# Optimization experiments

Measured on AMD Instinct MI355X. Metric: run time of the kernel, lower is better.

Reference implementation:

```python
import jax, jax.numpy as jnp
import numpy as np

EPS_BN = 1e-5

def _conv1x1(x, w, b):
    # x: [B,C,N], w: [O,C], b: [O] -> [B,O,N]
    return jnp.einsum('oc,bcn->bon', w, x) + b[:, None]

def _bn(x, g, b):
    # BatchNorm1d in training mode: batch stats over (B, N), biased variance
    mu = jnp.mean(x, axis=(0, 2), keepdims=True)
    var = jnp.var(x, axis=(0, 2), keepdims=True)
    return g[:, None] * (x - mu) / jnp.sqrt(var + EPS_BN) + b[:, None]

def _lrelu(x):
    return jnp.where(x >= 0, x, 0.2 * x)

def setup_inputs() -> dict:
    key = jax.random.key(0)
    B, N, S = 4, 16384, 2048
    D1, D2, FINT = 128, 256, 64
    IN, M1, M2 = D1 + D2, 256, 128
    ks = jax.random.split(key, 20)
    def rn(k, shape, scale=1.0):
        return jax.random.normal(k, shape, dtype=jnp.float32) * scale
    return {
        'xyz1': rn(ks[0], (B, 3, N)),
        'xyz2': rn(ks[1], (B, 3, S)),
        'points1': rn(ks[2], (B, D1, N)),
        'points2': rn(ks[3], (B, D2, S)),
        'conv1_w': rn(ks[4], (M1, IN), 0.05), 'conv1_b': rn(ks[5], (M1,), 0.05),
        'bn1_g': jnp.ones((M1,), jnp.float32), 'bn1_b': jnp.zeros((M1,), jnp.float32),
        'conv2_w': rn(ks[6], (M2, M1), 0.05), 'conv2_b': rn(ks[7], (M2,), 0.05),
        'bn2_g': jnp.ones((M2,), jnp.float32), 'bn2_b': jnp.zeros((M2,), jnp.float32),
        'wg_w': rn(ks[8], (FINT, D2), 0.05), 'wg_b': rn(ks[9], (FINT,), 0.05),
        'wg_bn_g': jnp.ones((FINT,), jnp.float32), 'wg_bn_b': jnp.zeros((FINT,), jnp.float32),
        'wx_w': rn(ks[10], (FINT, D1), 0.05), 'wx_b': rn(ks[11], (FINT,), 0.05),
        'wx_bn_g': jnp.ones((FINT,), jnp.float32), 'wx_bn_b': jnp.zeros((FINT,), jnp.float32),
        'psi_w': rn(ks[12], (1, FINT), 0.05), 'psi_b': rn(ks[13], (1,), 0.05),
        'psi_bn_g': jnp.ones((1,), jnp.float32), 'psi_bn_b': jnp.zeros((1,), jnp.float32),
    }

def reference(xyz1, xyz2, points1, points2,
              conv1_w, conv1_b, bn1_g, bn1_b,
              conv2_w, conv2_b, bn2_g, bn2_b,
              wg_w, wg_b, wg_bn_g, wg_bn_b,
              wx_w, wx_b, wx_bn_g, wx_bn_b,
              psi_w, psi_b, psi_bn_g, psi_bn_b):
    x1 = xyz1.transpose(0, 2, 1)        # [B,N,3]
    x2 = xyz2.transpose(0, 2, 1)        # [B,S,3]
    p2 = points2.transpose(0, 2, 1)     # [B,S,D2]
    # squared euclidean distances [B,N,S]
    d = (jnp.sum(x1 * x1, -1)[:, :, None]
         + jnp.sum(x2 * x2, -1)[:, None, :]
         - 2.0 * jnp.einsum('bnc,bsc->bns', x1, x2))
    # 3 smallest distances (torch: full sort + slice [:3])
    neg, idx = jax.lax.top_k(-d, 3)     # idx: [B,N,3]
    d3 = -neg
    recip = 1.0 / (d3 + 1e-8)
    w = recip / jnp.sum(recip, -1, keepdims=True)  # [B,N,3]
    gathered = jax.vmap(lambda p, i: p[i])(p2, idx)  # [B,N,3,D2]
    interp = jnp.einsum('bnkd,bnk->bnd', gathered, w)  # [B,N,D2]
    interp_t = interp.transpose(0, 2, 1)               # [B,D2,N]
    # attention gate: g = interpolated, x = points1
    g1 = _bn(_conv1x1(interp_t, wg_w, wg_b), wg_bn_g, wg_bn_b)
    xx1 = _bn(_conv1x1(points1, wx_w, wx_b), wx_bn_g, wx_bn_b)
    psi = jax.nn.sigmoid(_bn(_conv1x1(_lrelu(g1 + xx1), psi_w, psi_b), psi_bn_g, psi_bn_b))
    p1 = points1 * psi                                  # [B,D1,N]
    new = jnp.concatenate([p1, interp_t], axis=1)       # [B,D1+D2,N]
    new = _lrelu(_bn(_conv1x1(new, conv1_w, conv1_b), bn1_g, bn1_b))
    new = _lrelu(_bn(_conv1x1(new, conv2_w, conv2_b), bn2_g, bn2_b))
    return new
```

## Files before the change

### kernel.cpp

```cpp
#include <hip/hip_runtime.h>
#include <hip/hip_bf16.h>

#define Bq    4
#define NPTS  16384
#define SPTS  2048
#define NCH   8
#define SCH   (SPTS/NCH)
#define CNTF  65536.0f
#define BNEPS 1e-5f

typedef unsigned short u16t;
typedef unsigned int   u32t;
typedef __attribute__((ext_vector_type(8))) short s16x8;
typedef __attribute__((ext_vector_type(4))) float f32x4;

#define AS1(p) ((const __attribute__((address_space(1))) void*)(p))
#define AS3(p) ((__attribute__((address_space(3))) void*)(p))

__device__ __forceinline__ float b2f(u16t u){
  union { u32t i; float f; } v; v.i = ((u32t)u) << 16; return v.f;
}
__device__ __forceinline__ u16t f2b(float f){
  __hip_bfloat16 h = __float2bfloat16(f);
  return *reinterpret_cast<u16t*>(&h);
}
__device__ __forceinline__ float lrelu(float x){ return x >= 0.0f ? x : 0.2f*x; }

#define ST_WG  0
#define ST_WX  128
#define ST_PSI 256
#define ST_BN1 272
#define ST_BN2 784

#define WOFF_C1 0
#define WOFF_C2 98304
#define WOFF_WG 131072
#define WOFF_WX 147456
#define WTOTAL  155648

#define O_STATS  0u
#define O_WB     8192u
#define O_PSIPRE 319488u
#define O_P2T    581632u
#define O_PART   O_P2T
#define O_P1T    4775936u
#define O_INT    21553152u
#define O_H1     55107584u
#define O_PD     O_H1
#define O_PI     (O_H1 + 6291456u)
#define O_IDX3   (O_H1 + 12582912u)
#define O_W3     (O_H1 + 13369344u)
#define O_YG     O_H1
#define O_YX     (O_H1 + 8388608u)
#define O_H2     O_INT

__global__ __launch_bounds__(256) void knn_part_kernel(const float* __restrict__ xyz1, const float* __restrict__ xyz2,
                                                       float* __restrict__ pd, int* __restrict__ pi){
  __shared__ float4 sp[SCH];
  const int b = blockIdx.z;
  const int c = blockIdx.y;
  const int t = threadIdx.x;
  {
    int s = c*SCH + t;
    float x = xyz2[(b*3+0)*SPTS+s];
    float y = xyz2[(b*3+1)*SPTS+s];
    float z = xyz2[(b*3+2)*SPTS+s];
    sp[t] = make_float4(x, y, z, x*x+y*y+z*z);
  }
  __syncthreads();
  const int n = blockIdx.x*256 + t;
  float px = xyz1[(b*3+0)*NPTS+n];
  float py = xyz1[(b*3+1)*NPTS+n];
  float pz = xyz1[(b*3+2)*NPTS+n];
  float s1 = px*px+py*py+pz*pz;
  float d0=3.4e38f, d1=3.4e38f, d2=3.4e38f;
  int   i0=0, i1=0, i2=0;
  for (int s=0; s<SCH; ++s){
    float4 q = sp[s];
    float dot = fmaf(pz, q.z, fmaf(py, q.y, px*q.x));
    float key = (s1 + q.w) - 2.0f*dot;
    if (key < d2){
      int gi = c*SCH + s;
      if (key < d1){
        if (key < d0){ d2=d1; i2=i1; d1=d0; i1=i0; d0=key; i0=gi; }
        else         { d2=d1; i2=i1; d1=key; i1=gi; }
      } else         { d2=key; i2=gi; }
    }
  }
  size_t base = (((size_t)b*NPTS + n)*NCH + c)*3;
  pd[base]=d0; pd[base+1]=d1; pd[base+2]=d2;
  pi[base]=i0; pi[base+1]=i1; pi[base+2]=i2;
}

__global__ __launch_bounds__(256) void knn_merge_kernel(const float* __restrict__ pd, const int* __restrict__ pi,
                                                        int* __restrict__ idx3, float* __restrict__ w3){
  const int p = blockIdx.x*256 + threadIdx.x;
  const float* dp = pd + (size_t)p*NCH*3;
  const int*   ip = pi + (size_t)p*NCH*3;
  float d0=3.4e38f, d1=3.4e38f, d2=3.4e38f;
  int   i0=0, i1=0, i2=0;
  #pragma unroll
  for (int k=0; k<NCH*3; ++k){
    float key = dp[k]; int gi = ip[k];
    if (key < d2){
      if (key < d1){
        if (key < d0){ d2=d1; i2=i1; d1=d0; i1=i0; d0=key; i0=gi; }
        else         { d2=d1; i2=i1; d1=key; i1=gi; }
      } else         { d2=key; i2=gi; }
    }
  }
  float r0=1.0f/(d0+1e-8f), r1=1.0f/(d1+1e-8f), r2=1.0f/(d2+1e-8f);
  float rs = r0+r1+r2;
  size_t base = (size_t)p*3;
  idx3[base]=i0; idx3[base+1]=i1; idx3[base+2]=i2;
  w3[base]=r0/rs; w3[base+1]=r1/rs; w3[base+2]=r2/rs;
}

template<int C, int NN>
__global__ __launch_bounds__(256) void tpose_kernel(const float* __restrict__ src, u16t* __restrict__ dst){
  __shared__ float tile[64][65];
  const int n0 = blockIdx.x * 64;
  const int c0 = blockIdx.y * 64;
  const int b  = blockIdx.z;
  const int t  = threadIdx.x;
  #pragma unroll
  for (int i = 0; i < 16; ++i){
    int idx = t + i*256;
    int cc = idx >> 6, nn = idx & 63;
    tile[cc][nn] = src[((size_t)b*C + c0 + cc)*NN + n0 + nn];
  }
  __syncthreads();
  #pragma unroll
  for (int i = 0; i < 16; ++i){
    int idx = t + i*256;
    int nn = idx >> 6, cc = idx & 63;
    dst[((size_t)b*NN + n0 + nn)*C + c0 + cc] = f2b(tile[cc][nn]);
  }
}

__global__ __launch_bounds__(256) void wcvt_kernel(const float* __restrict__ w1, const float* __restrict__ w2,
                                                   const float* __restrict__ wg, const float* __restrict__ wx,
                                                   u16t* __restrict__ wb){
  int i = blockIdx.x*256 + threadIdx.x;
  if (i >= WTOTAL) return;
  float v;
  if      (i < WOFF_C2) v = w1[i];
  else if (i < WOFF_WG) v = w2[i - WOFF_C2];
  else if (i < WOFF_WX) v = wg[i - WOFF_WG];
  else                  v = wx[i - WOFF_WX];
  wb[i] = f2b(v);
}

__global__ __launch_bounds__(256) void interp_kernel(const u16t* __restrict__ p2t, const int* __restrict__ idx3,
                                                     const float* __restrict__ w3, u16t* __restrict__ it){
  const int t = threadIdx.x;
  const int pid = blockIdx.x*8 + (t >> 5);
  const int l = t & 31;
  const int b = pid >> 14;
  size_t pb = (size_t)pid*3;
  int i0 = idx3[pb], i1 = idx3[pb+1], i2 = idx3[pb+2];
  float w0 = w3[pb], w1 = w3[pb+1], w2 = w3[pb+2];
  const u16t* r0 = p2t + ((size_t)b*SPTS + i0)*256 + l*8;
  const u16t* r1 = p2t + ((size_t)b*SPTS + i1)*256 + l*8;
  const u16t* r2 = p2t + ((size_t)b*SPTS + i2)*256 + l*8;
  uint4 q0 = *reinterpret_cast<const uint4*>(r0);
  uint4 q1 = *reinterpret_cast<const uint4*>(r1);
  uint4 q2 = *reinterpret_cast<const uint4*>(r2);
  const u32t* a0 = reinterpret_cast<const u32t*>(&q0);
  const u32t* a1 = reinterpret_cast<const u32t*>(&q1);
  const u32t* a2 = reinterpret_cast<const u32t*>(&q2);
  u32t ow[4];
  #pragma unroll
  for (int j = 0; j < 4; ++j){
    u32t u0 = a0[j], u1 = a1[j], u2 = a2[j];
    float lo = fmaf(w2, b2f((u16t)u2), fmaf(w1, b2f((u16t)u1), w0*b2f((u16t)u0)));
    float hi = fmaf(w2, b2f((u16t)(u2>>16)), fmaf(w1, b2f((u16t)(u1>>16)), w0*b2f((u16t)(u0>>16))));
    ow[j] = (u32t)f2b(lo) | ((u32t)f2b(hi) << 16);
  }
  *reinterpret_cast<uint4*>(it + (size_t)pid*256 + l*8) = make_uint4(ow[0], ow[1], ow[2], ow[3]);
}

template<int CIN, int OUT, bool SPLIT>
__global__ __launch_bounds__(256, 1) void mfma_conv_kernel(const u16t* __restrict__ xa, const u16t* __restrict__ xb,
                                                           const u16t* __restrict__ W, const float* __restrict__ bias,
                                                           u16t* __restrict__ y, float* __restrict__ partial){
  constexpr int MW = OUT/4;
  constexpr int MF = MW/16;
  constexpr int NC = CIN/64;
  __shared__ u16t sbuf[2][64*64];
  const int bid = blockIdx.x;
  const int b = bid >> 8;
  const int n0 = (bid & 255) * 64;
  const int wv = threadIdx.x >> 6;
  const int lane = threadIdx.x & 63;
  const int lr = lane & 15;
  const int kg = lane >> 4;
  const int m0 = wv * MW;

  f32x4 acc[MF][4];
  #pragma unroll
  for (int mf = 0; mf < MF; ++mf)
    #pragma unroll
    for (int nf = 0; nf < 4; ++nf){ acc[mf][nf][0]=0.f; acc[mf][nf][1]=0.f; acc[mf][nf][2]=0.f; acc[mf][nf][3]=0.f; }

  const u16t* wrow[MF];
  #pragma unroll
  for (int mf = 0; mf < MF; ++mf)
    wrow[mf] = W + (size_t)(m0 + mf*16 + lr)*CIN + kg*8;

  const int prow0 = wv*16 + (lane>>3);
  const int gslot = (lane & 7) ^ ((lane >> 3) & 7);
  int rdoff[2][4];
  #pragma unroll
  for (int ks = 0; ks < 2; ++ks)
    #pragma unroll
    for (int nf = 0; nf < 4; ++nf)
      rdoff[ks][nf] = (nf*16 + lr)*64 + (((ks*4 + kg) ^ (lr & 7)) << 3);

  auto stage = [&](int c, int buf){
    #pragma unroll
    for (int i = 0; i < 2; ++i){
      int p = prow0 + i*8;
      const u16t* g;
      if (SPLIT){
        if (c < 2) g = xa + ((size_t)b*NPTS + n0 + p)*128 + c*64     + gslot*8;
        else       g = xb + ((size_t)b*NPTS + n0 + p)*256 + (c-2)*64 + gslot*8;
      } else {
        g = xa + ((size_t)b*NPTS + n0 + p)*CIN + c*64 + gslot*8;
      }
      u16t* l = &sbuf[buf][(wv*16 + i*8)*64];
      __builtin_amdgcn_global_load_lds(AS1(g), AS3(l), 16, 0, 0);
    }
  };

  stage(0, 0);
  __syncthreads();
  #pragma unroll
  for (int c = 0; c < NC; ++c){
    if (c + 1 < NC) stage(c+1, (c+1)&1);
    #pragma unroll
    for (int ks = 0; ks < 2; ++ks){
      const int k0 = c*2 + ks;
      s16x8 av[MF];
      #pragma unroll
      for (int mf = 0; mf < MF; ++mf)
        av[mf] = *reinterpret_cast<const s16x8*>(wrow[mf] + k0*32);
      s16x8 bv[4];
      #pragma unroll
      for (int nf = 0; nf < 4; ++nf)
        bv[nf] = *reinterpret_cast<const s16x8*>(&sbuf[c&1][rdoff[ks][nf]]);
      #pragma unroll
      for (int mf = 0; mf < MF; ++mf)
        #pragma unroll
        for (int nf = 0; nf < 4; ++nf)
          acc[mf][nf] = __builtin_amdgcn_mfma_f32_16x16x32_bf16(av[mf], bv[nf], acc[mf][nf], 0, 0, 0);
    }
    __syncthreads();
  }

  #pragma unroll
  for (int mf = 0; mf < MF; ++mf){
    int mb = m0 + mf*16 + kg*4;
    float4 bs = *reinterpret_cast<const float4*>(bias + mb);
    float s0=0.f,s1=0.f,s2=0.f,s3=0.f,q0=0.f,q1=0.f,q2=0.f,q3=0.f;
    #pragma unroll
    for (int nf = 0; nf < 4; ++nf){
      int n = n0 + nf*16 + lr;
      float v0 = acc[mf][nf][0] + bs.x;
      float v1 = acc[mf][nf][1] + bs.y;
      float v2 = acc[mf][nf][2] + bs.z;
      float v3 = acc[mf][nf][3] + bs.w;
      s0+=v0; q0+=v0*v0; s1+=v1; q1+=v1*v1;
      s2+=v2; q2+=v2*v2; s3+=v3; q3+=v3*v3;
      uint2 pv;
      pv.x = (u32t)f2b(v0) | ((u32t)f2b(v1) << 16);
      pv.y = (u32t)f2b(v2) | ((u32t)f2b(v3) << 16);
      *reinterpret_cast<uint2*>(y + ((size_t)b*NPTS + n)*OUT + mb) = pv;
    }
    #pragma unroll
    for (int o = 1; o < 16; o <<= 1){
      s0 += __shfl_xor(s0, o); s1 += __shfl_xor(s1, o);
      s2 += __shfl_xor(s2, o); s3 += __shfl_xor(s3, o);
      q0 += __shfl_xor(q0, o); q1 += __shfl_xor(q1, o);
      q2 += __shfl_xor(q2, o); q3 += __shfl_xor(q3, o);
    }
    if (lr == 0){
      float* pp = partial + (size_t)bid*(OUT*2) + mb*2;
      pp[0]=s0; pp[1]=q0; pp[2]=s1; pp[3]=q1;
      pp[4]=s2; pp[5]=q2; pp[6]=s3; pp[7]=q3;
    }
  }
}

template<int E>
__global__ __launch_bounds__(256) void reduce_stats_kernel(const float* __restrict__ p, float* __restrict__ st){
  __shared__ float ls[8][32];
  const int t = threadIdx.x;
  const int kq = t >> 5, es = t & 31;
  const int e = blockIdx.x*32 + es;
  float s = 0.f;
  const float* pp = p + (size_t)kq*128*E + e;
  #pragma unroll 16
  for (int i = 0; i < 128; ++i) s += pp[(size_t)i*E];
  ls[kq][es] = s;
  __syncthreads();
  if (kq == 0){
    st[e] = ((ls[0][es]+ls[1][es])+(ls[2][es]+ls[3][es]))
          + ((ls[4][es]+ls[5][es])+(ls[6][es]+ls[7][es]));
  }
}

__global__ __launch_bounds__(256) void gate_kernel(const u16t* __restrict__ yg, const u16t* __restrict__ yx,
                                                   const float* __restrict__ stg, const float* __restrict__ stx,
                                                   const float* __restrict__ wg_bn_g, const float* __restrict__ wg_bn_b,
                                                   const float* __restrict__ wx_bn_g, const float* __restrict__ wx_bn_b,
                                                   const float* __restrict__ psi_w, const float* __restrict__ psi_b,
                                                   float* __restrict__ psipre, float* __restrict__ stpsi){
  __shared__ float lag[64], lbg[64], lax[64], lbx[64], lpw[64];
  __shared__ float red[8];
  const int t = threadIdx.x;
  if (t < 64){
    float m  = stg[t*2] * (1.0f/CNTF);
    float vv = fmaxf(stg[t*2+1]*(1.0f/CNTF) - m*m, 0.0f);
    float iv = 1.0f/sqrtf(vv + BNEPS);
    float gm = wg_bn_g[t];
    lag[t] = gm*iv; lbg[t] = wg_bn_b[t] - m*gm*iv;
    m  = stx[t*2] * (1.0f/CNTF);
    vv = fmaxf(stx[t*2+1]*(1.0f/CNTF) - m*m, 0.0f);
    iv = 1.0f/sqrtf(vv + BNEPS);
    gm = wx_bn_g[t];
    lax[t] = gm*iv; lbx[t] = wx_bn_b[t] - m*gm*iv;
    lpw[t] = psi_w[t];
  }
  __syncthreads();
  const int p = blockIdx.x*256 + t;
  const u16t* rg = yg + (size_t)p*64;
  const u16t* rx = yx + (size_t)p*64;
  float acc = psi_b[0];
  #pragma unroll
  for (int u = 0; u < 8; ++u){
    uint4 qg = *reinterpret_cast<const uint4*>(rg + u*8);
    uint4 qx = *reinterpret_cast<const uint4*>(rx + u*8);
    const u32t* g4 = reinterpret_cast<const u32t*>(&qg);
    const u32t* x4 = reinterpret_cast<const u32t*>(&qx);
    #pragma unroll
    for (int e = 0; e < 4; ++e){
      int j = u*8 + e*2;
      float gv0 = fmaf(b2f((u16t)g4[e]),        lag[j],   lbg[j]);
      float xv0 = fmaf(b2f((u16t)x4[e]),        lax[j],   lbx[j]);
      float gv1 = fmaf(b2f((u16t)(g4[e]>>16)),  lag[j+1], lbg[j+1]);
      float xv1 = fmaf(b2f((u16t)(x4[e]>>16)),  lax[j+1], lbx[j+1]);
      acc = fmaf(lpw[j],   lrelu(gv0 + xv0), acc);
      acc = fmaf(lpw[j+1], lrelu(gv1 + xv1), acc);
    }
  }
  psipre[p] = acc;
  float s = acc, q = acc*acc;
  #pragma unroll
  for (int o = 32; o; o >>= 1){ s += __shfl_xor(s, o); q += __shfl_xor(q, o); }
  if ((t & 63) == 0){ red[(t>>6)*2] = s; red[(t>>6)*2+1] = q; }
  __syncthreads();
  if (t == 0){
    atomicAdd(&stpsi[0], red[0]+red[2]+red[4]+red[6]);
    atomicAdd(&stpsi[1], red[1]+red[3]+red[5]+red[7]);
  }
}

__global__ __launch_bounds__(256) void scale_p1_kernel(u16t* __restrict__ p1t, const float* __restrict__ psipre,
                                                       const float* __restrict__ stpsi,
                                                       const float* __restrict__ psi_bn_g, const float* __restrict__ psi_bn_b){
  const int p = blockIdx.x*256 + threadIdx.x;
  float m  = stpsi[0]*(1.0f/CNTF);
  float vv = fmaxf(stpsi[1]*(1.0f/CNTF) - m*m, 0.0f);
  float iv = 1.0f/sqrtf(vv + BNEPS);
  float ap = psi_bn_g[0]*iv;
  float bp = psi_bn_b[0] - m*ap;
  float z  = fmaf(psipre[p], ap, bp);
  float psi = 1.0f/(1.0f + expf(-z));
  u16t* r = p1t + (size_t)p*128;
  #pragma unroll
  for (int u = 0; u < 16; ++u){
    uint4 q = *reinterpret_cast<uint4*>(r + u*8);
    u32t* a = reinterpret_cast<u32t*>(&q);
    #pragma unroll
    for (int j = 0; j < 4; ++j){
      float lo = b2f((u16t)a[j]) * psi;
      float hi = b2f((u16t)(a[j]>>16)) * psi;
      a[j] = (u32t)f2b(lo) | ((u32t)f2b(hi) << 16);
    }
    *reinterpret_cast<uint4*>(r + u*8) = q;
  }
}

__global__ __launch_bounds__(256) void bnrelu256_kernel(u16t* __restrict__ x, const float* __restrict__ st,
                                                        const float* __restrict__ g, const float* __restrict__ bb){
  __shared__ float sa[256], sc[256];
  const int t = threadIdx.x;
  {
    float m  = st[t*2]*(1.0f/CNTF);
    float vv = fmaxf(st[t*2+1]*(1.0f/CNTF) - m*m, 0.0f);
    float iv = 1.0f/sqrtf(vv + BNEPS);
    float gm = g[t];
    sa[t] = gm*iv; sc[t] = bb[t] - m*gm*iv;
  }
  __syncthreads();
  size_t e4 = ((size_t)blockIdx.x*256 + t)*4;
  int c0 = (int)(e4 & 255);
  uint2 v = *reinterpret_cast<uint2*>(x + e4);
  float f0 = lrelu(fmaf(b2f((u16t)v.x),        sa[c0],   sc[c0]));
  float f1 = lrelu(fmaf(b2f((u16t)(v.x>>16)),  sa[c0+1], sc[c0+1]));
  float f2 = lrelu(fmaf(b2f((u16t)v.y),        sa[c0+2], sc[c0+2]));
  float f3 = lrelu(fmaf(b2f((u16t)(v.y>>16)),  sa[c0+3], sc[c0+3]));
  v.x = (u32t)f2b(f0) | ((u32t)f2b(f1) << 16);
  v.y = (u32t)f2b(f2) | ((u32t)f2b(f3) << 16);
  *reinterpret_cast<uint2*>(x + e4) = v;
}

__global__ __launch_bounds__(256) void final_kernel(const u16t* __restrict__ h2, const float* __restrict__ st,
                                                    const float* __restrict__ g, const float* __restrict__ bb,
                                                    float* __restrict__ out){
  __shared__ float am[128], cm[128];
  __shared__ float tile[64][129];
  const int t = threadIdx.x;
  if (t < 128){
    float m  = st[t*2]*(1.0f/CNTF);
    float vv = fmaxf(st[t*2+1]*(1.0f/CNTF) - m*m, 0.0f);
    float iv = 1.0f/sqrtf(vv + BNEPS);
    float gm = g[t];
    am[t] = gm*iv; cm[t] = bb[t] - m*gm*iv;
  }
  __syncthreads();
  const int n0 = blockIdx.x * 64;
  const int b  = blockIdx.y;
  #pragma unroll
  for (int i = 0; i < 32; ++i){
    int idx = t + i*256;
    int mm = idx & 127, nn = idx >> 7;
    float v = fmaf(b2f(h2[((size_t)b*NPTS + n0 + nn)*128 + mm]), am[mm], cm[mm]);
    tile[nn][mm] = lrelu(v);
  }
  __syncthreads();
  #pragma unroll
  for (int i = 0; i < 32; ++i){
    int idx = t + i*256;
    int nn = idx & 63, mm = idx >> 6;
    out[((size_t)(b*128 + mm))*NPTS + n0 + nn] = tile[nn][mm];
  }
}

extern "C" void kernel_launch(void* const* d_in, const int* in_sizes, int n_in,
                              void* d_out, int out_size, void* d_ws, size_t ws_size,
                              hipStream_t stream){
  const float* xyz1    = (const float*)d_in[0];
  const float* xyz2    = (const float*)d_in[1];
  const float* points1 = (const float*)d_in[2];
  const float* points2 = (const float*)d_in[3];
  const float* conv1_w = (const float*)d_in[4];
  const float* conv1_b = (const float*)d_in[5];
  const float* bn1_g   = (const float*)d_in[6];
  const float* bn1_b   = (const float*)d_in[7];
  const float* conv2_w = (const float*)d_in[8];
  const float* conv2_b = (const float*)d_in[9];
  const float* bn2_g   = (const float*)d_in[10];
  const float* bn2_b   = (const float*)d_in[11];
  const float* wg_w    = (const float*)d_in[12];
  const float* wg_b    = (const float*)d_in[13];
  const float* wg_bn_g = (const float*)d_in[14];
  const float* wg_bn_b = (const float*)d_in[15];
  const float* wx_w    = (const float*)d_in[16];
  const float* wx_b    = (const float*)d_in[17];
  const float* wx_bn_g = (const float*)d_in[18];
  const float* wx_bn_b = (const float*)d_in[19];
  const float* psi_w   = (const float*)d_in[20];
  const float* psi_b   = (const float*)d_in[21];
  const float* psi_bn_g= (const float*)d_in[22];
  const float* psi_bn_b= (const float*)d_in[23];

  char* ws = (char*)d_ws;
  float* stats  = (float*)(ws + O_STATS);
  u16t*  wb     = (u16t*)(ws + O_WB);
  float* psipre = (float*)(ws + O_PSIPRE);
  u16t*  p2t    = (u16t*)(ws + O_P2T);
  float* part   = (float*)(ws + O_PART);
  u16t*  p1t    = (u16t*)(ws + O_P1T);
  u16t*  itp    = (u16t*)(ws + O_INT);
  u16t*  h1t    = (u16t*)(ws + O_H1);
  float* pd     = (float*)(ws + O_PD);
  int*   pi     = (int*)(ws + O_PI);
  int*   idx3   = (int*)(ws + O_IDX3);
  float* w3     = (float*)(ws + O_W3);
  u16t*  ygt    = (u16t*)(ws + O_YG);
  u16t*  yxt    = (u16t*)(ws + O_YX);
  u16t*  h2t    = (u16t*)(ws + O_H2);

  hipMemsetAsync(ws + O_STATS, 0, 8192, stream);

  knn_part_kernel<<<dim3(NPTS/256, NCH, Bq), 256, 0, stream>>>(xyz1, xyz2, pd, pi);
  knn_merge_kernel<<<(Bq*NPTS)/256, 256, 0, stream>>>(pd, pi, idx3, w3);
  tpose_kernel<256, SPTS><<<dim3(SPTS/64, 4, Bq), 256, 0, stream>>>(points2, p2t);
  interp_kernel<<<(Bq*NPTS)/8, 256, 0, stream>>>(p2t, idx3, w3, itp);
  tpose_kernel<128, NPTS><<<dim3(NPTS/64, 2, Bq), 256, 0, stream>>>(points1, p1t);
  wcvt_kernel<<<(WTOTAL+255)/256, 256, 0, stream>>>(conv1_w, conv2_w, wg_w, wx_w, wb);

  mfma_conv_kernel<256, 64, false><<<Bq*(NPTS/64), 256, 0, stream>>>(itp, nullptr, wb+WOFF_WG, wg_b, ygt, part);
  reduce_stats_kernel<128><<<4, 256, 0, stream>>>(part, stats+ST_WG);
  mfma_conv_kernel<128, 64, false><<<Bq*(NPTS/64), 256, 0, stream>>>(p1t, nullptr, wb+WOFF_WX, wx_b, yxt, part);
  reduce_stats_kernel<128><<<4, 256, 0, stream>>>(part, stats+ST_WX);
  gate_kernel<<<256, 256, 0, stream>>>(ygt, yxt, stats+ST_WG, stats+ST_WX,
                                       wg_bn_g, wg_bn_b, wx_bn_g, wx_bn_b,
                                       psi_w, psi_b, psipre, stats+ST_PSI);
  scale_p1_kernel<<<256, 256, 0, stream>>>(p1t, psipre, stats+ST_PSI, psi_bn_g, psi_bn_b);

  mfma_conv_kernel<384, 256, true><<<Bq*(NPTS/64), 256, 0, stream>>>(p1t, itp, wb+WOFF_C1, conv1_b, h1t, part);
  reduce_stats_kernel<512><<<16, 256, 0, stream>>>(part, stats+ST_BN1);
  bnrelu256_kernel<<<16384, 256, 0, stream>>>(h1t, stats+ST_BN1, bn1_g, bn1_b);

  mfma_conv_kernel<256, 128, false><<<Bq*(NPTS/64), 256, 0, stream>>>(h1t, nullptr, wb+WOFF_C2, conv2_b, h2t, part);
  reduce_stats_kernel<256><<<8, 256, 0, stream>>>(part, stats+ST_BN2);
  final_kernel<<<dim3(NPTS/64, Bq), 256, 0, stream>>>(h2t, stats+ST_BN2, bn2_g, bn2_b, (float*)d_out);
}
```

Measured before the change: 241.0 us.

## Fold psi gating into conv1 accumulators and make KNN top-3 branchless

Removes the scale_p1 kernel, which rescaled the points1 buffer in place. The psi sigmoid is now computed inside the conv1 MFMA kernel and applied to the accumulators once the first 128 input channels (the points1 half) have been accumulated, exploiting the fact that psi is a per-column scale. The KNN partial and merge kernels replace nested branches with a branchless select/fmed3 top-3 update. A separate prep kernel precomputes the xyz2 float4 table, which knn_part now reads from global memory instead of LDS. The fused psi scale saves a full read/write pass over p1t, but it multiplies fp32 partial sums rather than bf16-rounded inputs, and global reads in the inner KNN loop may cost more than LDS broadcast.

```diff
diff --git a/kernel.cpp b/kernel.cpp
--- a/kernel.cpp
+++ b/kernel.cpp
@@ -41,6 +41,7 @@
 #define O_STATS  0u
 #define O_WB     8192u
 #define O_PSIPRE 319488u
+#define O_SP     O_PSIPRE
 #define O_P2T    581632u
 #define O_PART   O_P2T
 #define O_P1T    4775936u
@@ -54,38 +55,42 @@
 #define O_YX     (O_H1 + 8388608u)
 #define O_H2     O_INT
 
-__global__ __launch_bounds__(256) void knn_part_kernel(const float* __restrict__ xyz1, const float* __restrict__ xyz2,
+__global__ __launch_bounds__(256) void knn_prep_kernel(const float* __restrict__ xyz2, float4* __restrict__ sp){
+  int i = blockIdx.x*256 + threadIdx.x;
+  int b = i >> 11, s = i & (SPTS-1);
+  float x = xyz2[(b*3+0)*SPTS+s];
+  float y = xyz2[(b*3+1)*SPTS+s];
+  float z = xyz2[(b*3+2)*SPTS+s];
+  sp[i] = make_float4(x, y, z, x*x+y*y+z*z);
+}
+
+__global__ __launch_bounds__(256) void knn_part_kernel(const float* __restrict__ xyz1, const float4* __restrict__ sp,
                                                        float* __restrict__ pd, int* __restrict__ pi){
-  __shared__ float4 sp[SCH];
   const int b = blockIdx.z;
   const int c = blockIdx.y;
-  const int t = threadIdx.x;
-  {
-    int s = c*SCH + t;
-    float x = xyz2[(b*3+0)*SPTS+s];
-    float y = xyz2[(b*3+1)*SPTS+s];
-    float z = xyz2[(b*3+2)*SPTS+s];
-    sp[t] = make_float4(x, y, z, x*x+y*y+z*z);
-  }
-  __syncthreads();
-  const int n = blockIdx.x*256 + t;
+  const int n = blockIdx.x*256 + threadIdx.x;
+  const float4* cp = sp + (size_t)b*SPTS + c*SCH;
   float px = xyz1[(b*3+0)*NPTS+n];
   float py = xyz1[(b*3+1)*NPTS+n];
   float pz = xyz1[(b*3+2)*NPTS+n];
   float s1 = px*px+py*py+pz*pz;
   float d0=3.4e38f, d1=3.4e38f, d2=3.4e38f;
   int   i0=0, i1=0, i2=0;
+  const int cbase = c*SCH;
+  #pragma unroll 8
   for (int s=0; s<SCH; ++s){
-    float4 q = sp[s];
+    float4 q = cp[s];
     float dot = fmaf(pz, q.z, fmaf(py, q.y, px*q.x));
     float key = (s1 + q.w) - 2.0f*dot;
-    if (key < d2){
-      int gi = c*SCH + s;
-      if (key < d1){
-        if (key < d0){ d2=d1; i2=i1; d1=d0; i1=i0; d0=key; i0=gi; }
-        else         { d2=d1; i2=i1; d1=key; i1=gi; }
-      } else         { d2=key; i2=gi; }
-    }
+    int gi = cbase + s;
+    bool c0 = key < d0, c1 = key < d1, c2 = key < d2;
+    int ni2 = c1 ? i1 : (c2 ? gi : i2);
+    int ni1 = c0 ? i0 : (c1 ? gi : i1);
+    i0 = c0 ? gi : i0;
+    float nd2 = fminf(d2, fmaxf(d1, key));
+    d1 = __builtin_amdgcn_fmed3f(d0, d1, key);
+    d0 = fminf(d0, key);
+    d2 = nd2; i1 = ni1; i2 = ni2;
   }
   size_t base = (((size_t)b*NPTS + n)*NCH + c)*3;
   pd[base]=d0; pd[base+1]=d1; pd[base+2]=d2;
@@ -102,12 +107,14 @@
   #pragma unroll
   for (int k=0; k<NCH*3; ++k){
     float key = dp[k]; int gi = ip[k];
-    if (key < d2){
-      if (key < d1){
-        if (key < d0){ d2=d1; i2=i1; d1=d0; i1=i0; d0=key; i0=gi; }
-        else         { d2=d1; i2=i1; d1=key; i1=gi; }
-      } else         { d2=key; i2=gi; }
-    }
+    bool c0 = key < d0, c1 = key < d1, c2 = key < d2;
+    int ni2 = c1 ? i1 : (c2 ? gi : i2);
+    int ni1 = c0 ? i0 : (c1 ? gi : i1);
+    i0 = c0 ? gi : i0;
+    float nd2 = fminf(d2, fmaxf(d1, key));
+    d1 = __builtin_amdgcn_fmed3f(d0, d1, key);
+    d0 = fminf(d0, key);
+    d2 = nd2; i1 = ni1; i2 = ni2;
   }
   float r0=1.0f/(d0+1e-8f), r1=1.0f/(d1+1e-8f), r2=1.0f/(d2+1e-8f);
   float rs = r0+r1+r2;
@@ -183,7 +190,9 @@
 template<int CIN, int OUT, bool SPLIT>
 __global__ __launch_bounds__(256, 1) void mfma_conv_kernel(const u16t* __restrict__ xa, const u16t* __restrict__ xb,
                                                            const u16t* __restrict__ W, const float* __restrict__ bias,
-                                                           u16t* __restrict__ y, float* __restrict__ partial){
+                                                           u16t* __restrict__ y, float* __restrict__ partial,
+                                                           const float* __restrict__ psipre, const float* __restrict__ stpsi,
+                                                           const float* __restrict__ pbn_g, const float* __restrict__ pbn_b){
   constexpr int MW = OUT/4;
   constexpr int MF = MW/16;
   constexpr int NC = CIN/64;
@@ -196,6 +205,20 @@
   const int lr = lane & 15;
   const int kg = lane >> 4;
   const int m0 = wv * MW;
+
+  float psiv[4];
+  if (SPLIT){
+    float m  = stpsi[0]*(1.0f/CNTF);
+    float vv = fmaxf(stpsi[1]*(1.0f/CNTF) - m*m, 0.0f);
+    float iv = 1.0f/sqrtf(vv + BNEPS);
+    float ap = pbn_g[0]*iv;
+    float bp = pbn_b[0] - m*ap;
+    #pragma unroll
+    for (int nf = 0; nf < 4; ++nf){
+      float z = fmaf(psipre[b*NPTS + n0 + nf*16 + lr], ap, bp);
+      psiv[nf] = 1.0f/(1.0f + expf(-z));
+    }
+  }
 
   f32x4 acc[MF][4];
   #pragma unroll
@@ -254,6 +277,15 @@
         #pragma unroll
         for (int nf = 0; nf < 4; ++nf)
           acc[mf][nf] = __builtin_amdgcn_mfma_f32_16x16x32_bf16(av[mf], bv[nf], acc[mf][nf], 0, 0, 0);
+    }
+    if (SPLIT && c == 1){
+      #pragma unroll
+      for (int mf = 0; mf < MF; ++mf)
+        #pragma unroll
+        for (int nf = 0; nf < 4; ++nf){
+          acc[mf][nf][0] *= psiv[nf]; acc[mf][nf][1] *= psiv[nf];
+          acc[mf][nf][2] *= psiv[nf]; acc[mf][nf][3] *= psiv[nf];
+        }
     }
     __syncthreads();
   }
@@ -363,32 +395,6 @@
   if (t == 0){
     atomicAdd(&stpsi[0], red[0]+red[2]+red[4]+red[6]);
     atomicAdd(&stpsi[1], red[1]+red[3]+red[5]+red[7]);
-  }
-}
-
-__global__ __launch_bounds__(256) void scale_p1_kernel(u16t* __restrict__ p1t, const float* __restrict__ psipre,
-                                                       const float* __restrict__ stpsi,
-                                                       const float* __restrict__ psi_bn_g, const float* __restrict__ psi_bn_b){
-  const int p = blockIdx.x*256 + threadIdx.x;
-  float m  = stpsi[0]*(1.0f/CNTF);
-  float vv = fmaxf(stpsi[1]*(1.0f/CNTF) - m*m, 0.0f);
-  float iv = 1.0f/sqrtf(vv + BNEPS);
-  float ap = psi_bn_g[0]*iv;
-  float bp = psi_bn_b[0] - m*ap;
-  float z  = fmaf(psipre[p], ap, bp);
-  float psi = 1.0f/(1.0f + expf(-z));
-  u16t* r = p1t + (size_t)p*128;
-  #pragma unroll
-  for (int u = 0; u < 16; ++u){
-    uint4 q = *reinterpret_cast<uint4*>(r + u*8);
-    u32t* a = reinterpret_cast<u32t*>(&q);
-    #pragma unroll
-    for (int j = 0; j < 4; ++j){
-      float lo = b2f((u16t)a[j]) * psi;
-      float hi = b2f((u16t)(a[j]>>16)) * psi;
-      a[j] = (u32t)f2b(lo) | ((u32t)f2b(hi) << 16);
-    }
-    *reinterpret_cast<uint4*>(r + u*8) = q;
   }
 }
 
@@ -480,6 +486,7 @@
   float* stats  = (float*)(ws + O_STATS);
   u16t*  wb     = (u16t*)(ws + O_WB);
   float* psipre = (float*)(ws + O_PSIPRE);
+  float4* sp    = (float4*)(ws + O_SP);
   u16t*  p2t    = (u16t*)(ws + O_P2T);
   float* part   = (float*)(ws + O_PART);
   u16t*  p1t    = (u16t*)(ws + O_P1T);
@@ -495,27 +502,31 @@
 
   hipMemsetAsync(ws + O_STATS, 0, 8192, stream);
 
-  knn_part_kernel<<<dim3(NPTS/256, NCH, Bq), 256, 0, stream>>>(xyz1, xyz2, pd, pi);
+  knn_prep_kernel<<<(Bq*SPTS)/256, 256, 0, stream>>>(xyz2, sp);
+  knn_part_kernel<<<dim3(NPTS/256, NCH, Bq), 256, 0, stream>>>(xyz1, sp, pd, pi);
   knn_merge_kernel<<<(Bq*NPTS)/256, 256, 0, stream>>>(pd, pi, idx3, w3);
   tpose_kernel<256, SPTS><<<dim3(SPTS/64, 4, Bq), 256, 0, stream>>>(points2, p2t);
   interp_kernel<<<(Bq*NPTS)/8, 256, 0, stream>>>(p2t, idx3, w3, itp);
   tpose_kernel<128, NPTS><<<dim3(NPTS/64, 2, Bq), 256, 0, stream>>>(points1, p1t);
   wcvt_kernel<<<(WTOTAL+255)/256, 256, 0, stream>>>(conv1_w, conv2_w, wg_w, wx_w, wb);
 
-  mfma_conv_kernel<256, 64, false><<<Bq*(NPTS/64), 256, 0, stream>>>(itp, nullptr, wb+WOFF_WG, wg_b, ygt, part);
+  mfma_conv_kernel<256, 64, false><<<Bq*(NPTS/64), 256, 0, stream>>>(itp, nullptr, wb+WOFF_WG, wg_b, ygt, part,
+                                                                     nullptr, nullptr, nullptr, nullptr);
   reduce_stats_kernel<128><<<4, 256, 0, stream>>>(part, stats+ST_WG);
-  mfma_conv_kernel<128, 64, false><<<Bq*(NPTS/64), 256, 0, stream>>>(p1t, nullptr, wb+WOFF_WX, wx_b, yxt, part);
+  mfma_conv_kernel<128, 64, false><<<Bq*(NPTS/64), 256, 0, stream>>>(p1t, nullptr, wb+WOFF_WX, wx_b, yxt, part,
+                                                                     nullptr, nullptr, nullptr, nullptr);
   reduce_stats_kernel<128><<<4, 256, 0, stream>>>(part, stats+ST_WX);
   gate_kernel<<<256, 256, 0, stream>>>(ygt, yxt, stats+ST_WG, stats+ST_WX,
                                        wg_bn_g, wg_bn_b, wx_bn_g, wx_bn_b,
                                        psi_w, psi_b, psipre, stats+ST_PSI);
-  scale_p1_kernel<<<256, 256, 0, stream>>>(p1t, psipre, stats+ST_PSI, psi_bn_g, psi_bn_b);
-
-  mfma_conv_kernel<384, 256, true><<<Bq*(NPTS/64), 256, 0, stream>>>(p1t, itp, wb+WOFF_C1, conv1_b, h1t, part);
+
+  mfma_conv_kernel<384, 256, true><<<Bq*(NPTS/64), 256, 0, stream>>>(p1t, itp, wb+WOFF_C1, conv1_b, h1t, part,
+                                                                     psipre, stats+ST_PSI, psi_bn_g, psi_bn_b);
   reduce_stats_kernel<512><<<16, 256, 0, stream>>>(part, stats+ST_BN1);
   bnrelu256_kernel<<<16384, 256, 0, stream>>>(h1t, stats+ST_BN1, bn1_g, bn1_b);
 
-  mfma_conv_kernel<256, 128, false><<<Bq*(NPTS/64), 256, 0, stream>>>(h1t, nullptr, wb+WOFF_C2, conv2_b, h2t, part);
+  mfma_conv_kernel<256, 128, false><<<Bq*(NPTS/64), 256, 0, stream>>>(h1t, nullptr, wb+WOFF_C2, conv2_b, h2t, part,
+                                                                      nullptr, nullptr, nullptr, nullptr);
   reduce_stats_kernel<256><<<8, 256, 0, stream>>>(part, stats+ST_BN2);
   final_kernel<<<dim3(NPTS/64, Bq), 256, 0, stream>>>(h2t, stats+ST_BN2, bn2_g, bn2_b, (float*)d_out);
 }
```

Result: faster. 226.3 us (-6.1%).
